# Optimization experiments

Measured on AMD Instinct MI355X. Metric: run time of the kernel, lower is better.

The kernel has to match this reference:

```python
import jax, jax.numpy as jnp
import numpy as np

EPS = 1e-5

def rmsnorm(x, g):
    var = jnp.mean(jnp.square(x), axis=-1, keepdims=True)
    return x * jax.lax.rsqrt(var + EPS) * g

def setup_inputs() -> dict:
    key = jax.random.key(0)
    ks = jax.random.split(key, 8)
    B, S, T, D = 2, 2048, 2048, 1024
    H, HKV, HD = 16, 4, 64
    std = 0.02
    return {
        "x": jax.random.normal(ks[0], (B, S, D), jnp.float32),
        "kv": jax.random.normal(ks[1], (B, T, D), jnp.float32),
        "wq": jax.random.normal(ks[2], (H * HD, D), jnp.float32) * std,
        "wk": jax.random.normal(ks[3], (HKV * HD, D), jnp.float32) * std,
        "wv": jax.random.normal(ks[4], (HKV * HD, D), jnp.float32) * std,
        "wo": jax.random.normal(ks[5], (D, H * HD), jnp.float32) * std,
        "gq": jnp.ones((D,), jnp.float32),
        "gkv": jnp.ones((D,), jnp.float32),
    }

def reference(x, kv, wq, wk, wv, wo, gq, gkv):
    B, S, D = x.shape
    T = kv.shape[1]
    H, HKV, HD = 16, 4, 64
    R = H // HKV  # heads per kv group
    xn = rmsnorm(x, gq)
    kvn = rmsnorm(kv, gkv)
    # projections
    q = (xn @ wq.T).reshape(B, S, HKV, R, HD)   # grouped query heads
    k = (kvn @ wk.T).reshape(B, T, HKV, HD)
    v = (kvn @ wv.T).reshape(B, T, HKV, HD)
    scale = 1.0 / jnp.sqrt(jnp.float32(HD))
    # block-mask is None -> full dense cross attention; GQA via broadcast einsum
    scores = jnp.einsum('bsgrd,btgd->bgrst', q, k) * scale  # [B,HKV,R,S,T]
    probs = jax.nn.softmax(scores, axis=-1)
    out = jnp.einsum('bgrst,btgd->bsgrd', probs, v)  # [B,S,HKV,R,HD]
    out = out.reshape(B, S, H * HD) @ wo.T
    return x + out
```

## Files before the change

### kernel.cpp

```cpp
#include <hip/hip_runtime.h>

#define DEV __device__ __forceinline__

typedef __attribute__((ext_vector_type(8))) _Float16 h8;
typedef __attribute__((ext_vector_type(4))) float f32x4;
typedef __fp16 __attribute__((ext_vector_type(2))) hh2;

DEV unsigned short f2h(float f) {
  union { _Float16 h[2]; unsigned short u[2]; } v;
  v.h[0] = (_Float16)f;
  return v.u[0];
}

DEV float h2f(unsigned short u) {
  union { _Float16 h[2]; unsigned short u[2]; } v;
  v.u[0] = u;
  return (float)v.h[0];
}

DEV void async_load16(const void* g, void* l) {
  __builtin_amdgcn_global_load_lds(
      (const __attribute__((address_space(1))) void*)g,
      (__attribute__((address_space(3))) void*)l,
      16, 0, 0);
}


__global__ __launch_bounds__(256) void prep(const float* __restrict__ x,
                                            const float* __restrict__ kv,
                                            const float* __restrict__ wq,
                                            const float* __restrict__ wk,
                                            const float* __restrict__ wv,
                                            const float* __restrict__ wo,
                                            const float* __restrict__ gq,
                                            const float* __restrict__ gkv,
                                            unsigned short* __restrict__ wqb,
                                            unsigned short* __restrict__ wkvb,
                                            unsigned short* __restrict__ wob,
                                            unsigned short* __restrict__ xn,
                                            unsigned short* __restrict__ kvn,
                                            float qscale) {
  const int b = blockIdx.x, tid = threadIdx.x;
  if (b < 2560) {
    const float* src;
    unsigned short* dst;
    float sc = 1.0f;
    int base;
    if (b < 1024) { src = wq; dst = wqb; sc = qscale; base = b; }
    else if (b < 1280) { src = wk; dst = wkvb; base = b - 1024; }
    else if (b < 1536) { src = wv; dst = wkvb + 262144; base = b - 1280; }
    else { src = wo; dst = wob; base = b - 1536; }
    const int i = (base * 256 + tid) * 4;
    float4 v = *(const float4*)&src[i];
    ushort4 o;
    o.x = f2h(v.x * sc); o.y = f2h(v.y * sc);
    o.z = f2h(v.z * sc); o.w = f2h(v.w * sc);
    *(ushort4*)&dst[i] = o;
    return;
  }
  int row = b - 2560;
  const float* src;
  const float* g;
  unsigned short* dst;
  if (row < 4096) { src = x; g = gq; dst = xn; }
  else { row -= 4096; src = kv; g = gkv; dst = kvn; }
  const float* xr = src + (size_t)row * 1024;
  float4 v = *(const float4*)&xr[tid * 4];
  float ss = v.x * v.x + v.y * v.y + v.z * v.z + v.w * v.w;
  ss += __shfl_xor(ss, 32); ss += __shfl_xor(ss, 16);
  ss += __shfl_xor(ss, 8);  ss += __shfl_xor(ss, 4);
  ss += __shfl_xor(ss, 2);  ss += __shfl_xor(ss, 1);
  __shared__ float red[4];
  if ((tid & 63) == 0) red[tid >> 6] = ss;
  __syncthreads();
  float tot = red[0] + red[1] + red[2] + red[3];
  float inv = rsqrtf(tot * (1.0f / 1024.0f) + 1e-5f);
  float4 gv = *(const float4*)&g[tid * 4];
  ushort4 o;
  o.x = f2h(v.x * inv * gv.x); o.y = f2h(v.y * inv * gv.y);
  o.z = f2h(v.z * inv * gv.z); o.w = f2h(v.w * inv * gv.w);
  *(ushort4*)&dst[(size_t)row * 1024 + tid * 4] = o;
}

__global__ __launch_bounds__(256) void proj_gemm(const unsigned short* __restrict__ xn,
                                                 const unsigned short* __restrict__ kvn,
                                                 const unsigned short* __restrict__ wqb,
                                                 const unsigned short* __restrict__ wkvb,
                                                 unsigned short* __restrict__ qb,
                                                 unsigned short* __restrict__ kb,
                                                 unsigned short* __restrict__ vTb) {
  __shared__ unsigned short Al[2][2][128 * 32];
  __shared__ unsigned short Bl[2][2][64 * 32];
  const int tid = threadIdx.x;
  const int w = tid >> 6, l = tid & 63;
  const int quad = l >> 4, ln = l & 15;
  const int wm0 = (w >> 1) * 64, wn0 = (w & 1) * 32;
  const int r4 = l >> 2;
  const int c4s = (((l & 3) ^ ((l >> 3) & 3))) * 8;
  const int qs8 = (quad ^ ((l >> 1) & 3)) * 8;

  int z = blockIdx.x;
  const unsigned short *A, *W;
  int m0, n0, isq;
  if (z < 512) {
    A = xn; W = wqb; isq = 1;
    m0 = (((z >> 7) << 3) + (z & 7)) * 128;
    n0 = ((z >> 3) & 15) * 64;
  } else {
    z -= 512; A = kvn; W = wkvb; isq = 0;
    m0 = (((z >> 6) << 3) + (z & 7)) * 128;
    n0 = ((z >> 3) & 7) * 64;
  }

  f32x4 acc[4][2] = {};

  auto stage = [&](int buf, int kk) {
#pragma unroll
    for (int j = 0; j < 6; ++j) {
      const int idx = w * 6 + j;
      if (idx < 16) {
        const int p = idx >> 3, rb = (idx & 7) * 16;
        async_load16(A + (size_t)(m0 + rb + r4) * 1024 + kk + p * 32 + c4s,
                     &Al[buf][p][rb * 32]);
      } else {
        const int ib = idx - 16;
        const int p = ib >> 2, rb = (ib & 3) * 16;
        async_load16(W + (size_t)(n0 + rb + r4) * 1024 + kk + p * 32 + c4s,
                     &Bl[buf][p][rb * 32]);
      }
    }
  };

  stage(0, 0);
#pragma unroll 2
  for (int it = 0; it < 16; ++it) {
    const int buf = it & 1;
    __syncthreads();
    if (it < 15) stage(buf ^ 1, (it + 1) * 64);
#pragma unroll
    for (int kc = 0; kc < 2; ++kc) {
      h8 af[4], bf[2];
#pragma unroll
      for (int mi = 0; mi < 4; ++mi)
        af[mi] = *(const h8*)&Al[buf][kc][(wm0 + mi * 16 + ln) * 32 + qs8];
#pragma unroll
      for (int ni = 0; ni < 2; ++ni)
        bf[ni] = *(const h8*)&Bl[buf][kc][(wn0 + ni * 16 + ln) * 32 + qs8];
#pragma unroll
      for (int mi = 0; mi < 4; ++mi)
#pragma unroll
        for (int ni = 0; ni < 2; ++ni)
          acc[mi][ni] = __builtin_amdgcn_mfma_f32_16x16x32_f16(af[mi], bf[ni], acc[mi][ni], 0, 0, 0);
    }
  }

#pragma unroll
  for (int mi = 0; mi < 4; ++mi)
#pragma unroll
    for (int ni = 0; ni < 2; ++ni)
#pragma unroll
      for (int r = 0; r < 4; ++r) {
        const int row = m0 + wm0 + mi * 16 + quad * 4 + r;
        const int col = n0 + wn0 + ni * 16 + ln;
        const unsigned short v = f2h(acc[mi][ni][r]);
        if (isq) {
          qb[((size_t)row << 10) + col] = v;
        } else if (col < 256) {
          kb[(size_t)row * 256 + col] = v;
        } else {
          const int c2 = col - 256, gg = c2 >> 6, dd = c2 & 63;
          const int bb = row >> 11, t = row & 2047;
          vTb[((size_t)((bb * 4 + gg) * 64 + dd) << 11) + t] = v;
        }
      }
}

__global__ __launch_bounds__(256) void o_gemm(const unsigned short* __restrict__ O0,
                                              const unsigned short* __restrict__ O1,
                                              const float* __restrict__ l0p,
                                              const float* __restrict__ l1p,
                                              const unsigned short* __restrict__ wob,
                                              const float* __restrict__ x,
                                              float* __restrict__ out) {
  __shared__ unsigned short Al[2][2][128 * 32];
  __shared__ unsigned short Bl[2][2][64 * 32];
  __shared__ float Linv[16 * 128];
  const int tid = threadIdx.x;
  const int w = tid >> 6, l = tid & 63;
  const int quad = l >> 4, ln = l & 15;
  const int wm0 = (w >> 1) * 64, wn0 = (w & 1) * 32;
  const int r4 = l >> 2;
  const int c4s = (((l & 3) ^ ((l >> 3) & 3))) * 8;
  const int qs8 = (quad ^ ((l >> 1) & 3)) * 8;

  const int z = blockIdx.x;
  const int m0 = (((z >> 7) << 3) + (z & 7)) * 128;
  const int n0 = ((z >> 3) & 15) * 64;

  {
    const int h = tid >> 4, r0 = (tid & 15) * 8;
#pragma unroll
    for (int i = 0; i < 8; ++i) {
      const int r = r0 + i;
      const size_t li = (size_t)(m0 + r) * 16 + h;
      Linv[h * 128 + r] = 1.0f / (l0p[li] + l1p[li]);
    }
  }
  __syncthreads();

  const int srow = tid >> 3;
  const int sp = (tid >> 2) & 1;
  const int ss = tid & 3;

  auto stageA = [&](int buf, int kk) {
    const int h = kk >> 6;
#pragma unroll
    for (int ps = 0; ps < 4; ++ps) {
      const int row = ps * 32 + srow;
      const size_t gidx = (size_t)(m0 + row) * 1024 + kk + sp * 32 + ss * 8;
      h8 a0 = *(const h8*)&O0[gidx];
      h8 a1 = *(const h8*)&O1[gidx];
      const _Float16 lv = (_Float16)Linv[h * 128 + row];
      h8 sum = a0 + a1;
#pragma unroll
      for (int q2 = 0; q2 < 8; ++q2) sum[q2] *= lv;
      const int sl = ss ^ ((row >> 1) & 3);
      *(h8*)&Al[buf][sp][row * 32 + sl * 8] = sum;
    }
  };
  auto stageB = [&](int buf, int kk) {
#pragma unroll
    for (int j = 0; j < 2; ++j) {
      const int ib = w * 2 + j;
      const int p = ib >> 2, rb = (ib & 3) * 16;
      async_load16(wob + (size_t)(n0 + rb + r4) * 1024 + kk + p * 32 + c4s,
                   &Bl[buf][p][rb * 32]);
    }
  };

  f32x4 acc[4][2] = {};
  stageB(0, 0);
  stageA(0, 0);
  for (int it = 0; it < 16; ++it) {
    const int buf = it & 1;
    __syncthreads();
    if (it < 15) { stageB(buf ^ 1, (it + 1) * 64); stageA(buf ^ 1, (it + 1) * 64); }
#pragma unroll
    for (int kc = 0; kc < 2; ++kc) {
      h8 af[4], bf[2];
#pragma unroll
      for (int mi = 0; mi < 4; ++mi)
        af[mi] = *(const h8*)&Al[buf][kc][(wm0 + mi * 16 + ln) * 32 + qs8];
#pragma unroll
      for (int ni = 0; ni < 2; ++ni)
        bf[ni] = *(const h8*)&Bl[buf][kc][(wn0 + ni * 16 + ln) * 32 + qs8];
#pragma unroll
      for (int mi = 0; mi < 4; ++mi)
#pragma unroll
        for (int ni = 0; ni < 2; ++ni)
          acc[mi][ni] = __builtin_amdgcn_mfma_f32_16x16x32_f16(af[mi], bf[ni], acc[mi][ni], 0, 0, 0);
    }
  }

#pragma unroll
  for (int mi = 0; mi < 4; ++mi)
#pragma unroll
    for (int ni = 0; ni < 2; ++ni)
#pragma unroll
      for (int r = 0; r < 4; ++r) {
        const int row = m0 + wm0 + mi * 16 + quad * 4 + r;
        const int col = n0 + wn0 + ni * 16 + ln;
        const size_t idx = ((size_t)row << 10) + col;
        out[idx] = x[idx] + acc[mi][ni][r];
      }
}

__global__ __launch_bounds__(256, 4) void flash_attn(const unsigned short* __restrict__ q,
                                                     const unsigned short* __restrict__ k,
                                                     const unsigned short* __restrict__ vT,
                                                     unsigned short* __restrict__ o0,
                                                     unsigned short* __restrict__ o1,
                                                     float* __restrict__ l0p,
                                                     float* __restrict__ l1p) {
  __shared__ unsigned short KV[4][64 * 32];
  __shared__ unsigned short P[4 * 32 * 72];

  const int tid = threadIdx.x;
  const int w = tid >> 6, l = tid & 63;
  const int quad = l >> 4, ln = l & 15;
  const int s0 = blockIdx.x * 128;
  const int h = blockIdx.y, g = h >> 2;
  const int b = blockIdx.z >> 1, ts = blockIdx.z & 1;
  const int tbase = ts << 10;

  unsigned short* Opart = ts ? o1 : o0;
  float* lpart = ts ? l1p : l0p;

  h8 qf[2][2];
#pragma unroll
  for (int nq = 0; nq < 2; ++nq)
#pragma unroll
    for (int c = 0; c < 2; ++c)
      qf[nq][c] = *(const h8*)&q[(((size_t)(b * 2048 + s0 + w * 32 + nq * 16 + ln)) << 10) +
                                 h * 64 + c * 32 + quad * 8];

  f32x4 oacc[2][4] = {};
  float lsum[2] = {0.0f, 0.0f};

  const unsigned short* kbase = k + ((size_t)(b * 2048)) * 256 + g * 64;
  const unsigned short* vbase = vT + (((size_t)(b * 4 + g) * 64) << 11);
  unsigned short* Pw = &P[w * 32 * 72];

  const int r4 = l >> 2;
  const int c4s = (((l & 3) ^ ((l >> 3) & 3))) * 8;
  const int qs8 = (quad ^ ((l >> 1) & 3)) * 8;

  const hh2 one2 = {(__fp16)1.0f, (__fp16)1.0f};

  for (int it = 0; it < 16; ++it) {
    const int t0 = tbase + it * 64;
    __syncthreads();
#pragma unroll
    for (int c = 0; c < 4; ++c) {
      const unsigned short* src;
      if (w < 2)
        src = kbase + (size_t)(t0 + c * 16 + r4) * 256 + w * 32 + c4s;
      else
        src = vbase + (((size_t)(c * 16 + r4)) << 11) + t0 + (w - 2) * 32 + c4s;
      async_load16(src, &KV[w][c * 512]);
    }
    __syncthreads();

    f32x4 st[2][4];
#pragma unroll
    for (int tb = 0; tb < 4; ++tb) {
      h8 ka = *(const h8*)&KV[0][tb * 512 + ln * 32 + qs8];
      h8 kb2 = *(const h8*)&KV[1][tb * 512 + ln * 32 + qs8];
#pragma unroll
      for (int nq = 0; nq < 2; ++nq) {
        f32x4 s = {};
        s = __builtin_amdgcn_mfma_f32_16x16x32_f16(ka, qf[nq][0], s, 0, 0, 0);
        s = __builtin_amdgcn_mfma_f32_16x16x32_f16(kb2, qf[nq][1], s, 0, 0, 0);
        st[nq][tb] = s;
      }
    }

#pragma unroll
    for (int nq = 0; nq < 2; ++nq) {
#pragma unroll
      for (int tb = 0; tb < 4; ++tb) {
        float p0 = __builtin_amdgcn_exp2f(st[nq][tb][0]);
        float p1 = __builtin_amdgcn_exp2f(st[nq][tb][1]);
        float p2 = __builtin_amdgcn_exp2f(st[nq][tb][2]);
        float p3 = __builtin_amdgcn_exp2f(st[nq][tb][3]);
        union { hh2 h2; unsigned int u; } pa, pb;
        pa.h2 = __builtin_amdgcn_cvt_pkrtz(p0, p1);
        pb.h2 = __builtin_amdgcn_cvt_pkrtz(p2, p3);
#if __has_builtin(__builtin_amdgcn_fdot2)
        lsum[nq] = __builtin_amdgcn_fdot2(pa.h2, one2, lsum[nq], false);
        lsum[nq] = __builtin_amdgcn_fdot2(pb.h2, one2, lsum[nq], false);
#else
        lsum[nq] += (p0 + p1) + (p2 + p3);
#endif
        uint2 pk; pk.x = pa.u; pk.y = pb.u;
        *(uint2*)&Pw[(nq * 16 + ln) * 72 + tb * 16 + quad * 4] = pk;
      }
    }

    asm volatile("s_waitcnt lgkmcnt(0)" ::: "memory");

#pragma unroll
    for (int c = 0; c < 2; ++c) {
      h8 pf0 = *(const h8*)&Pw[(0 * 16 + ln) * 72 + c * 32 + quad * 8];
      h8 pf1 = *(const h8*)&Pw[(1 * 16 + ln) * 72 + c * 32 + quad * 8];
#pragma unroll
      for (int cb = 0; cb < 4; ++cb) {
        h8 vb = *(const h8*)&KV[2 + c][cb * 512 + ln * 32 + qs8];
        oacc[0][cb] = __builtin_amdgcn_mfma_f32_16x16x32_f16(pf0, vb, oacc[0][cb], 0, 0, 0);
        oacc[1][cb] = __builtin_amdgcn_mfma_f32_16x16x32_f16(pf1, vb, oacc[1][cb], 0, 0, 0);
      }
    }
  }

#pragma unroll
  for (int nq = 0; nq < 2; ++nq) {
    lsum[nq] += __shfl_xor(lsum[nq], 16);
    lsum[nq] += __shfl_xor(lsum[nq], 32);
    if (l < 16)
      lpart[(size_t)(b * 2048 + s0 + w * 32 + nq * 16 + l) * 16 + h] = lsum[nq];
#pragma unroll
    for (int r = 0; r < 4; ++r) {
      const size_t row = (size_t)(b * 2048 + s0 + w * 32 + nq * 16 + quad * 4 + r);
#pragma unroll
      for (int cb = 0; cb < 4; ++cb)
        Opart[(row << 10) + h * 64 + cb * 16 + ln] = f2h(oacc[nq][cb][r]);
    }
  }
}

extern "C" void kernel_launch(void* const* d_in, const int* in_sizes, int n_in,
                              void* d_out, int out_size, void* d_ws, size_t ws_size,
                              hipStream_t stream) {
  const float* x   = (const float*)d_in[0];
  const float* kv  = (const float*)d_in[1];
  const float* wq  = (const float*)d_in[2];
  const float* wk  = (const float*)d_in[3];
  const float* wv  = (const float*)d_in[4];
  const float* wo  = (const float*)d_in[5];
  const float* gq  = (const float*)d_in[6];
  const float* gkv = (const float*)d_in[7];

  char* ws = (char*)d_ws;
  unsigned short* xn   = (unsigned short*)(ws);
  unsigned short* kvn  = (unsigned short*)(ws + 8388608);
  unsigned short* qb   = (unsigned short*)(ws + 16777216);
  unsigned short* kb   = (unsigned short*)(ws + 25165824);
  unsigned short* vTb  = (unsigned short*)(ws + 27262976);
  unsigned short* wqb  = (unsigned short*)(ws + 37748736);
  unsigned short* wkvb = (unsigned short*)(ws + 39845888);
  unsigned short* wob  = (unsigned short*)(ws + 40894464);
  unsigned short* Opart0 = xn;
  unsigned short* Opart1 = kvn;
  float* l0p = (float*)wqb;
  float* l1p = (float*)(ws + 37748736 + 262144);

  const float qscale = 0.18033688011112042f;

  prep<<<10752, 256, 0, stream>>>(x, kv, wq, wk, wv, wo, gq, gkv,
                                  wqb, wkvb, wob, xn, kvn, qscale);

  proj_gemm<<<768, 256, 0, stream>>>(xn, kvn, wqb, wkvb, qb, kb, vTb);

  flash_attn<<<dim3(16, 16, 4), 256, 0, stream>>>(qb, kb, vTb, Opart0, Opart1, l0p, l1p);

  o_gemm<<<512, 256, 0, stream>>>(Opart0, Opart1, l0p, l1p, wob, x, (float*)d_out);
}
```

Before: 190.9 us.

## Replace double-buffered K loops with larger single-buffer stages in GEMMs and attention

Both projection GEMMs drop their two-stage prefetch pipeline. Each now loads a 128-wide K slice into one buffer, syncs, then computes, which halves the number of barrier rounds. The attention kernel likewise stages 128 keys and values per iteration in bigger LDS tiles and processes them in two halves, with its occupancy hint lowered from 4 to 3 blocks. This cuts loop and barrier overhead, but global-memory latency is no longer hidden behind compute within a block and now relies on other resident blocks.

```diff
diff --git a/kernel.cpp b/kernel.cpp
--- a/kernel.cpp
+++ b/kernel.cpp
@@ -89,8 +89,8 @@
                                                  unsigned short* __restrict__ qb,
                                                  unsigned short* __restrict__ kb,
                                                  unsigned short* __restrict__ vTb) {
-  __shared__ unsigned short Al[2][2][128 * 32];
-  __shared__ unsigned short Bl[2][2][64 * 32];
+  __shared__ unsigned short Al[4][128 * 32];
+  __shared__ unsigned short Bl[4][64 * 32];
   const int tid = threadIdx.x;
   const int w = tid >> 6, l = tid & 63;
   const int quad = l >> 4, ln = l & 15;
@@ -114,38 +114,33 @@
 
   f32x4 acc[4][2] = {};
 
-  auto stage = [&](int buf, int kk) {
-#pragma unroll
-    for (int j = 0; j < 6; ++j) {
-      const int idx = w * 6 + j;
-      if (idx < 16) {
+  for (int it = 0; it < 8; ++it) {
+    const int kk = it * 128;
+    __syncthreads();
+#pragma unroll
+    for (int j = 0; j < 12; ++j) {
+      const int idx = w * 12 + j;
+      if (idx < 32) {
         const int p = idx >> 3, rb = (idx & 7) * 16;
         async_load16(A + (size_t)(m0 + rb + r4) * 1024 + kk + p * 32 + c4s,
-                     &Al[buf][p][rb * 32]);
+                     &Al[p][rb * 32]);
       } else {
-        const int ib = idx - 16;
+        const int ib = idx - 32;
         const int p = ib >> 2, rb = (ib & 3) * 16;
         async_load16(W + (size_t)(n0 + rb + r4) * 1024 + kk + p * 32 + c4s,
-                     &Bl[buf][p][rb * 32]);
-      }
-    }
-  };
-
-  stage(0, 0);
-#pragma unroll 2
-  for (int it = 0; it < 16; ++it) {
-    const int buf = it & 1;
-    __syncthreads();
-    if (it < 15) stage(buf ^ 1, (it + 1) * 64);
-#pragma unroll
-    for (int kc = 0; kc < 2; ++kc) {
+                     &Bl[p][rb * 32]);
+      }
+    }
+    __syncthreads();
+#pragma unroll
+    for (int kc = 0; kc < 4; ++kc) {
       h8 af[4], bf[2];
 #pragma unroll
       for (int mi = 0; mi < 4; ++mi)
-        af[mi] = *(const h8*)&Al[buf][kc][(wm0 + mi * 16 + ln) * 32 + qs8];
+        af[mi] = *(const h8*)&Al[kc][(wm0 + mi * 16 + ln) * 32 + qs8];
 #pragma unroll
       for (int ni = 0; ni < 2; ++ni)
-        bf[ni] = *(const h8*)&Bl[buf][kc][(wn0 + ni * 16 + ln) * 32 + qs8];
+        bf[ni] = *(const h8*)&Bl[kc][(wn0 + ni * 16 + ln) * 32 + qs8];
 #pragma unroll
       for (int mi = 0; mi < 4; ++mi)
 #pragma unroll
@@ -182,8 +177,8 @@
                                               const unsigned short* __restrict__ wob,
                                               const float* __restrict__ x,
                                               float* __restrict__ out) {
-  __shared__ unsigned short Al[2][2][128 * 32];
-  __shared__ unsigned short Bl[2][2][64 * 32];
+  __shared__ unsigned short Al[4][128 * 32];
+  __shared__ unsigned short Bl[4][64 * 32];
   __shared__ float Linv[16 * 128];
   const int tid = threadIdx.x;
   const int w = tid >> 6, l = tid & 63;
@@ -206,54 +201,51 @@
       Linv[h * 128 + r] = 1.0f / (l0p[li] + l1p[li]);
     }
   }
-  __syncthreads();
-
-  const int srow = tid >> 3;
-  const int sp = (tid >> 2) & 1;
-  const int ss = tid & 3;
-
-  auto stageA = [&](int buf, int kk) {
-    const int h = kk >> 6;
-#pragma unroll
-    for (int ps = 0; ps < 4; ++ps) {
-      const int row = ps * 32 + srow;
-      const size_t gidx = (size_t)(m0 + row) * 1024 + kk + sp * 32 + ss * 8;
-      h8 a0 = *(const h8*)&O0[gidx];
-      h8 a1 = *(const h8*)&O1[gidx];
-      const _Float16 lv = (_Float16)Linv[h * 128 + row];
-      h8 sum = a0 + a1;
-#pragma unroll
-      for (int q2 = 0; q2 < 8; ++q2) sum[q2] *= lv;
-      const int sl = ss ^ ((row >> 1) & 3);
-      *(h8*)&Al[buf][sp][row * 32 + sl * 8] = sum;
-    }
-  };
-  auto stageB = [&](int buf, int kk) {
-#pragma unroll
-    for (int j = 0; j < 2; ++j) {
-      const int ib = w * 2 + j;
+
+  const int rowt = tid >> 3;
+  const int s0_ = tid & 7;
+
+  f32x4 acc[4][2] = {};
+
+  for (int it = 0; it < 8; ++it) {
+    const int kk = it * 128;
+    __syncthreads();
+#pragma unroll
+    for (int j = 0; j < 4; ++j) {
+      const int ib = w * 4 + j;
       const int p = ib >> 2, rb = (ib & 3) * 16;
       async_load16(wob + (size_t)(n0 + rb + r4) * 1024 + kk + p * 32 + c4s,
-                   &Bl[buf][p][rb * 32]);
-    }
-  };
-
-  f32x4 acc[4][2] = {};
-  stageB(0, 0);
-  stageA(0, 0);
-  for (int it = 0; it < 16; ++it) {
-    const int buf = it & 1;
-    __syncthreads();
-    if (it < 15) { stageB(buf ^ 1, (it + 1) * 64); stageA(buf ^ 1, (it + 1) * 64); }
-#pragma unroll
-    for (int kc = 0; kc < 2; ++kc) {
+                   &Bl[p][rb * 32]);
+    }
+#pragma unroll
+    for (int ps = 0; ps < 4; ++ps) {
+      const int row = ps * 32 + rowt;
+#pragma unroll
+      for (int si = 0; si < 2; ++si) {
+        const int slot = s0_ + si * 8;
+        const int col = kk + slot * 8;
+        const int h = col >> 6;
+        const size_t gidx = (size_t)(m0 + row) * 1024 + col;
+        h8 a0 = *(const h8*)&O0[gidx];
+        h8 a1 = *(const h8*)&O1[gidx];
+        const _Float16 lv = (_Float16)Linv[h * 128 + row];
+        h8 sum = a0 + a1;
+#pragma unroll
+        for (int q2 = 0; q2 < 8; ++q2) sum[q2] *= lv;
+        const int p = slot >> 2, g = slot & 3;
+        *(h8*)&Al[p][row * 32 + (g ^ ((row >> 1) & 3)) * 8] = sum;
+      }
+    }
+    __syncthreads();
+#pragma unroll
+    for (int kc = 0; kc < 4; ++kc) {
       h8 af[4], bf[2];
 #pragma unroll
       for (int mi = 0; mi < 4; ++mi)
-        af[mi] = *(const h8*)&Al[buf][kc][(wm0 + mi * 16 + ln) * 32 + qs8];
+        af[mi] = *(const h8*)&Al[kc][(wm0 + mi * 16 + ln) * 32 + qs8];
 #pragma unroll
       for (int ni = 0; ni < 2; ++ni)
-        bf[ni] = *(const h8*)&Bl[buf][kc][(wn0 + ni * 16 + ln) * 32 + qs8];
+        bf[ni] = *(const h8*)&Bl[kc][(wn0 + ni * 16 + ln) * 32 + qs8];
 #pragma unroll
       for (int mi = 0; mi < 4; ++mi)
 #pragma unroll
@@ -275,14 +267,15 @@
       }
 }
 
-__global__ __launch_bounds__(256, 4) void flash_attn(const unsigned short* __restrict__ q,
+__global__ __launch_bounds__(256, 3) void flash_attn(const unsigned short* __restrict__ q,
                                                      const unsigned short* __restrict__ k,
                                                      const unsigned short* __restrict__ vT,
                                                      unsigned short* __restrict__ o0,
                                                      unsigned short* __restrict__ o1,
                                                      float* __restrict__ l0p,
                                                      float* __restrict__ l1p) {
-  __shared__ unsigned short KV[4][64 * 32];
+  __shared__ unsigned short Kl[2][128 * 32];
+  __shared__ unsigned short Vl[4][64 * 32];
   __shared__ unsigned short P[4 * 32 * 72];
 
   const int tid = threadIdx.x;
@@ -317,67 +310,75 @@
 
   const hh2 one2 = {(__fp16)1.0f, (__fp16)1.0f};
 
-  for (int it = 0; it < 16; ++it) {
-    const int t0 = tbase + it * 64;
-    __syncthreads();
-#pragma unroll
-    for (int c = 0; c < 4; ++c) {
-      const unsigned short* src;
-      if (w < 2)
-        src = kbase + (size_t)(t0 + c * 16 + r4) * 256 + w * 32 + c4s;
-      else
-        src = vbase + (((size_t)(c * 16 + r4)) << 11) + t0 + (w - 2) * 32 + c4s;
-      async_load16(src, &KV[w][c * 512]);
-    }
-    __syncthreads();
-
-    f32x4 st[2][4];
-#pragma unroll
-    for (int tb = 0; tb < 4; ++tb) {
-      h8 ka = *(const h8*)&KV[0][tb * 512 + ln * 32 + qs8];
-      h8 kb2 = *(const h8*)&KV[1][tb * 512 + ln * 32 + qs8];
+  for (int it = 0; it < 8; ++it) {
+    const int t0 = tbase + it * 128;
+    __syncthreads();
+    if (w < 2) {
+#pragma unroll
+      for (int c = 0; c < 8; ++c)
+        async_load16(kbase + (size_t)(t0 + c * 16 + r4) * 256 + w * 32 + c4s,
+                     &Kl[w][c * 512]);
+    } else {
+#pragma unroll
+      for (int c = 0; c < 8; ++c) {
+        const int p = (w - 2) * 2 + (c >> 2), cc = c & 3;
+        async_load16(vbase + (((size_t)(cc * 16 + r4)) << 11) + t0 + p * 32 + c4s,
+                     &Vl[p][cc * 512]);
+      }
+    }
+    __syncthreads();
+
+#pragma unroll
+    for (int half = 0; half < 2; ++half) {
+      f32x4 st[2][4];
+#pragma unroll
+      for (int tb = 0; tb < 4; ++tb) {
+        const int trow = half * 64 + tb * 16 + ln;
+        h8 ka = *(const h8*)&Kl[0][trow * 32 + qs8];
+        h8 kb2 = *(const h8*)&Kl[1][trow * 32 + qs8];
+#pragma unroll
+        for (int nq = 0; nq < 2; ++nq) {
+          f32x4 s = {};
+          s = __builtin_amdgcn_mfma_f32_16x16x32_f16(ka, qf[nq][0], s, 0, 0, 0);
+          s = __builtin_amdgcn_mfma_f32_16x16x32_f16(kb2, qf[nq][1], s, 0, 0, 0);
+          st[nq][tb] = s;
+        }
+      }
+
 #pragma unroll
       for (int nq = 0; nq < 2; ++nq) {
-        f32x4 s = {};
-        s = __builtin_amdgcn_mfma_f32_16x16x32_f16(ka, qf[nq][0], s, 0, 0, 0);
-        s = __builtin_amdgcn_mfma_f32_16x16x32_f16(kb2, qf[nq][1], s, 0, 0, 0);
-        st[nq][tb] = s;
-      }
-    }
-
-#pragma unroll
-    for (int nq = 0; nq < 2; ++nq) {
-#pragma unroll
-      for (int tb = 0; tb < 4; ++tb) {
-        float p0 = __builtin_amdgcn_exp2f(st[nq][tb][0]);
-        float p1 = __builtin_amdgcn_exp2f(st[nq][tb][1]);
-        float p2 = __builtin_amdgcn_exp2f(st[nq][tb][2]);
-        float p3 = __builtin_amdgcn_exp2f(st[nq][tb][3]);
-        union { hh2 h2; unsigned int u; } pa, pb;
-        pa.h2 = __builtin_amdgcn_cvt_pkrtz(p0, p1);
-        pb.h2 = __builtin_amdgcn_cvt_pkrtz(p2, p3);
+#pragma unroll
+        for (int tb = 0; tb < 4; ++tb) {
+          float p0 = __builtin_amdgcn_exp2f(st[nq][tb][0]);
+          float p1 = __builtin_amdgcn_exp2f(st[nq][tb][1]);
+          float p2 = __builtin_amdgcn_exp2f(st[nq][tb][2]);
+          float p3 = __builtin_amdgcn_exp2f(st[nq][tb][3]);
+          union { hh2 h2; unsigned int u; } pa, pb;
+          pa.h2 = __builtin_amdgcn_cvt_pkrtz(p0, p1);
+          pb.h2 = __builtin_amdgcn_cvt_pkrtz(p2, p3);
 #if __has_builtin(__builtin_amdgcn_fdot2)
-        lsum[nq] = __builtin_amdgcn_fdot2(pa.h2, one2, lsum[nq], false);
-        lsum[nq] = __builtin_amdgcn_fdot2(pb.h2, one2, lsum[nq], false);
+          lsum[nq] = __builtin_amdgcn_fdot2(pa.h2, one2, lsum[nq], false);
+          lsum[nq] = __builtin_amdgcn_fdot2(pb.h2, one2, lsum[nq], false);
 #else
-        lsum[nq] += (p0 + p1) + (p2 + p3);
+          lsum[nq] += (p0 + p1) + (p2 + p3);
 #endif
-        uint2 pk; pk.x = pa.u; pk.y = pb.u;
-        *(uint2*)&Pw[(nq * 16 + ln) * 72 + tb * 16 + quad * 4] = pk;
-      }
-    }
-
-    asm volatile("s_waitcnt lgkmcnt(0)" ::: "memory");
-
-#pragma unroll
-    for (int c = 0; c < 2; ++c) {
-      h8 pf0 = *(const h8*)&Pw[(0 * 16 + ln) * 72 + c * 32 + quad * 8];
-      h8 pf1 = *(const h8*)&Pw[(1 * 16 + ln) * 72 + c * 32 + quad * 8];
-#pragma unroll
-      for (int cb = 0; cb < 4; ++cb) {
-        h8 vb = *(const h8*)&KV[2 + c][cb * 512 + ln * 32 + qs8];
-        oacc[0][cb] = __builtin_amdgcn_mfma_f32_16x16x32_f16(pf0, vb, oacc[0][cb], 0, 0, 0);
-        oacc[1][cb] = __builtin_amdgcn_mfma_f32_16x16x32_f16(pf1, vb, oacc[1][cb], 0, 0, 0);
+          uint2 pk; pk.x = pa.u; pk.y = pb.u;
+          *(uint2*)&Pw[(nq * 16 + ln) * 72 + tb * 16 + quad * 4] = pk;
+        }
+      }
+
+      asm volatile("s_waitcnt lgkmcnt(0)" ::: "memory");
+
+#pragma unroll
+      for (int c = 0; c < 2; ++c) {
+        h8 pf0 = *(const h8*)&Pw[(0 * 16 + ln) * 72 + c * 32 + quad * 8];
+        h8 pf1 = *(const h8*)&Pw[(1 * 16 + ln) * 72 + c * 32 + quad * 8];
+#pragma unroll
+        for (int cb = 0; cb < 4; ++cb) {
+          h8 vb = *(const h8*)&Vl[half * 2 + c][cb * 512 + ln * 32 + qs8];
+          oacc[0][cb] = __builtin_amdgcn_mfma_f32_16x16x32_f16(pf0, vb, oacc[0][cb], 0, 0, 0);
+          oacc[1][cb] = __builtin_amdgcn_mfma_f32_16x16x32_f16(pf1, vb, oacc[1][cb], 0, 0, 0);
+        }
       }
     }
   }
```

Result: slower. 195.7 us (+2.5%).
